# Kernel optimization log

Hardware: AMD Instinct MI355X
Metric: run time of the kernel (lower is better)

## Reference

```python
import jax, jax.numpy as jnp
import numpy as np

DIM = 2048
N_HEADS = 16
HEAD_DIM = DIM // N_HEADS
WINDOW = 256
B, S = 2, 2048


def setup_inputs() -> dict:
    key = jax.random.key(0)
    kx, kq, kk, kv, ko = jax.random.split(key, 5)
    bound = 1.0 / np.sqrt(DIM)  # nn.Linear default init range
    x = jax.random.normal(kx, (B, S, DIM), dtype=jnp.float32)
    wq = jax.random.uniform(kq, (DIM, DIM), jnp.float32, -bound, bound)
    wk = jax.random.uniform(kk, (DIM, DIM), jnp.float32, -bound, bound)
    wv = jax.random.uniform(kv, (DIM, DIM), jnp.float32, -bound, bound)
    wo = jax.random.uniform(ko, (DIM, DIM), jnp.float32, -bound, bound)
    return {"x": x, "wq": wq, "wk": wk, "wv": wv, "wo": wo}


def reference(x, wq, wk, wv, wo):
    b, s, d = x.shape
    scale = HEAD_DIM ** -0.5
    # projections (torch Linear: y = x @ W.T)
    q = (x @ wq.T).reshape(b, s, N_HEADS, HEAD_DIM)
    k = (x @ wk.T).reshape(b, s, N_HEADS, HEAD_DIM)
    v = (x @ wv.T).reshape(b, s, N_HEADS, HEAD_DIM)
    # scores: [b, h, i, j]
    scores = jnp.einsum("bihd,bjhd->bhij", q, k) * scale
    # faithful mask: (all-ones, window cleared, then triu(1)) == mask iff j - i > window//2
    idx = jnp.arange(s)
    mask = (idx[None, :] - idx[:, None]) > (WINDOW // 2)  # [s, s] bool, True = masked
    scores = jnp.where(mask[None, None, :, :], -jnp.inf, scores)
    attn = jax.nn.softmax(scores, axis=-1)
    out = jnp.einsum("bhij,bjhd->bihd", attn, v).reshape(b, s, d)
    return out @ wo.T
```

## Files before the change

### kernel.cpp

```cpp
#include <hip/hip_runtime.h>
#include <stdint.h>
#include <stddef.h>

#define DIMN 2048
#define NH 16
#define HD 128
#define SEQ 2048
#define WIN 128

typedef __attribute__((ext_vector_type(4))) float f32x4;
typedef __attribute__((ext_vector_type(8))) short bf16x8;
typedef __attribute__((ext_vector_type(4))) int i32x4;

__device__ __forceinline__ unsigned short f2bf(float f) {
  union { float f; unsigned u; } v; v.f = f;
  unsigned r = v.u + 0x7FFFu + ((v.u >> 16) & 1u);
  return (unsigned short)(r >> 16);
}

__global__ void cast_bf16_kernel(const float* __restrict__ src,
                                 unsigned short* __restrict__ dst, int n4) {
  int i = blockIdx.x * blockDim.x + threadIdx.x;
  const int stride = gridDim.x * blockDim.x;
  for (; i < n4; i += stride) {
    float4 v = ((const float4*)src)[i];
    ushort4 o;
    o.x = f2bf(v.x); o.y = f2bf(v.y); o.z = f2bf(v.z); o.w = f2bf(v.w);
    ((ushort4*)dst)[i] = o;
  }
}

__global__ void cast4_bf16_kernel(const float* __restrict__ s0, const float* __restrict__ s1,
                                  const float* __restrict__ s2, const float* __restrict__ s3,
                                  unsigned short* __restrict__ dst, int n4) {
  const float* s = (blockIdx.y == 0) ? s0 : (blockIdx.y == 1) ? s1 : (blockIdx.y == 2) ? s2 : s3;
  unsigned short* d = dst + (size_t)blockIdx.y * 4194304;
  int i = blockIdx.x * blockDim.x + threadIdx.x;
  const int stride = gridDim.x * blockDim.x;
  for (; i < n4; i += stride) {
    float4 v = ((const float4*)s)[i];
    ushort4 o;
    o.x = f2bf(v.x); o.y = f2bf(v.y); o.z = f2bf(v.z); o.w = f2bf(v.w);
    ((ushort4*)d)[i] = o;
  }
}

__device__ __forceinline__ void gemm_mainloop_128(
    const unsigned short* __restrict__ A, const unsigned short* __restrict__ B,
    int m0, int n0,
    unsigned short (*As)[40], unsigned short (*Bs)[40],
    f32x4 acc[4][4]) {
  const int t = threadIdx.x;
  const int lane = t & 63, wid = t >> 6;
  const int c = lane & 15, g = lane >> 4;
  const int wr = wid >> 1, wc = wid & 1;
  const int sr = t >> 2;
  const int sc8 = (t & 3) * 8;

  const unsigned short* pa0 = A + (size_t)(m0 + sr) * DIMN + sc8;
  const unsigned short* pa1 = pa0 + (size_t)64 * DIMN;
  const unsigned short* pb0 = B + (size_t)(n0 + sr) * DIMN + sc8;
  const unsigned short* pb1 = pb0 + (size_t)64 * DIMN;

  i32x4 ra0 = *(const i32x4*)pa0;
  i32x4 ra1 = *(const i32x4*)pa1;
  i32x4 rb0 = *(const i32x4*)pb0;
  i32x4 rb1 = *(const i32x4*)pb1;

  for (int k0 = 0; k0 < DIMN; k0 += 32) {
    __syncthreads();
    *(i32x4*)&As[sr][sc8] = ra0;
    *(i32x4*)&As[sr + 64][sc8] = ra1;
    *(i32x4*)&Bs[sr][sc8] = rb0;
    *(i32x4*)&Bs[sr + 64][sc8] = rb1;
    __syncthreads();
    if (k0 + 32 < DIMN) {
      ra0 = *(const i32x4*)(pa0 + k0 + 32);
      ra1 = *(const i32x4*)(pa1 + k0 + 32);
      rb0 = *(const i32x4*)(pb0 + k0 + 32);
      rb1 = *(const i32x4*)(pb1 + k0 + 32);
    }
    bf16x8 af[4], bfv[4];
#pragma unroll
    for (int mi = 0; mi < 4; ++mi)
      af[mi] = *(const bf16x8*)&As[wr * 64 + mi * 16 + c][g * 8];
#pragma unroll
    for (int ni = 0; ni < 4; ++ni)
      bfv[ni] = *(const bf16x8*)&Bs[wc * 64 + ni * 16 + c][g * 8];
#pragma unroll
    for (int mi = 0; mi < 4; ++mi)
#pragma unroll
      for (int ni = 0; ni < 4; ++ni)
        acc[mi][ni] = __builtin_amdgcn_mfma_f32_16x16x32_bf16(
            af[mi], bfv[ni], acc[mi][ni], 0, 0, 0);
  }
}

__global__ __launch_bounds__(256, 2) void gemm_qkv_kernel(
    const unsigned short* __restrict__ Xb,
    const unsigned short* __restrict__ Wq,
    const unsigned short* __restrict__ Wk,
    const unsigned short* __restrict__ Wv,
    unsigned short* __restrict__ Qb,
    unsigned short* __restrict__ Kb,
    unsigned short* __restrict__ Vt) {
  __shared__ __attribute__((aligned(16))) unsigned short As[128][40];
  __shared__ __attribute__((aligned(16))) unsigned short Bs[128][40];
  const int z = blockIdx.z;
  const unsigned short* W = (z == 0) ? Wq : (z == 1) ? Wk : Wv;
  const int m0 = blockIdx.y * 128, n0 = blockIdx.x * 128;

  f32x4 acc[4][4];
  const f32x4 zv = {0.f, 0.f, 0.f, 0.f};
#pragma unroll
  for (int i = 0; i < 4; ++i)
#pragma unroll
    for (int j = 0; j < 4; ++j) acc[i][j] = zv;

  gemm_mainloop_128(Xb, W, m0, n0, As, Bs, acc);

  const int lane = threadIdx.x & 63, wid = threadIdx.x >> 6;
  const int c = lane & 15, g = lane >> 4;
  const int wr = wid >> 1, wc = wid & 1;
  unsigned short* Out01 = (z == 0) ? Qb : Kb;
#pragma unroll
  for (int mi = 0; mi < 4; ++mi) {
#pragma unroll
    for (int ni = 0; ni < 4; ++ni) {
      const int mrow = m0 + wr * 64 + mi * 16 + g * 4;
      const int ncol = n0 + wc * 64 + ni * 16 + c;
      const int h = ncol >> 7, d = ncol & 127;
      const int b = mrow >> 11, s = mrow & 2047;
      if (z < 2) {
#pragma unroll
        for (int j = 0; j < 4; ++j)
          Out01[((size_t)(b * NH + h) * SEQ + s + j) * HD + d] =
              f2bf(acc[mi][ni][j]);
      } else {
        ushort4 pk;
        pk.x = f2bf(acc[mi][ni][0]); pk.y = f2bf(acc[mi][ni][1]);
        pk.z = f2bf(acc[mi][ni][2]); pk.w = f2bf(acc[mi][ni][3]);
        *(ushort4*)&Vt[((size_t)(b * NH + h) * HD + d) * SEQ + s] = pk;
      }
    }
  }
}

__global__ __launch_bounds__(256, 2) void gemm_out_kernel(
    const unsigned short* __restrict__ Ab,
    const unsigned short* __restrict__ Wo,
    float* __restrict__ Cf) {
  __shared__ __attribute__((aligned(16))) unsigned short As[128][40];
  __shared__ __attribute__((aligned(16))) unsigned short Bs[128][40];
  const int m0 = blockIdx.y * 128, n0 = blockIdx.x * 128;

  f32x4 acc[4][4];
  const f32x4 zv = {0.f, 0.f, 0.f, 0.f};
#pragma unroll
  for (int i = 0; i < 4; ++i)
#pragma unroll
    for (int j = 0; j < 4; ++j) acc[i][j] = zv;

  gemm_mainloop_128(Ab, Wo, m0, n0, As, Bs, acc);

  const int lane = threadIdx.x & 63, wid = threadIdx.x >> 6;
  const int c = lane & 15, g = lane >> 4;
  const int wr = wid >> 1, wc = wid & 1;
#pragma unroll
  for (int mi = 0; mi < 4; ++mi) {
#pragma unroll
    for (int ni = 0; ni < 4; ++ni) {
      const int mrow = m0 + wr * 64 + mi * 16 + g * 4;
      const int ncol = n0 + wc * 64 + ni * 16 + c;
#pragma unroll
      for (int j = 0; j < 4; ++j)
        Cf[(size_t)(mrow + j) * DIMN + ncol] = acc[mi][ni][j];
    }
  }
}

__global__ __launch_bounds__(256, 2) void attn_kernel(
    const unsigned short* __restrict__ Qg,
    const unsigned short* __restrict__ Kg,
    const unsigned short* __restrict__ Vtg,
    unsigned short* __restrict__ Og) {
  __shared__ __attribute__((aligned(16))) unsigned short Ks[64 * 128];
  __shared__ __attribute__((aligned(16))) unsigned short Vs[128 * 64];
  __shared__ __attribute__((aligned(16))) unsigned short Ps[4 * 32 * 64];

  const int bh = blockIdx.x, qt = blockIdx.y;
  const int q0 = qt * 128;
  const int t = threadIdx.x, wid = t >> 6, lane = t & 63;
  const int c = lane & 15, g = lane >> 4;
  const int swc = c & 7;

  const unsigned short* Kbh = Kg + (size_t)bh * SEQ * HD;
  const unsigned short* Vbh = Vtg + (size_t)bh * HD * SEQ;

  bf16x8 qf[2][4];
#pragma unroll
  for (int mi = 0; mi < 2; ++mi) {
    const unsigned short* qb =
        Qg + ((size_t)bh * SEQ + q0 + wid * 32 + mi * 16 + c) * HD + g * 8;
#pragma unroll
    for (int kk = 0; kk < 4; ++kk) qf[mi][kk] = *(const bf16x8*)(qb + kk * 32);
  }

  f32x4 o[2][8];
  const f32x4 zv = {0.f, 0.f, 0.f, 0.f};
#pragma unroll
  for (int mi = 0; mi < 2; ++mi)
#pragma unroll
    for (int ni = 0; ni < 8; ++ni) o[mi][ni] = zv;
  float M[2][4], L[2][4];
#pragma unroll
  for (int mi = 0; mi < 2; ++mi)
#pragma unroll
    for (int j = 0; j < 4; ++j) { M[mi][j] = -1e30f; L[mi][j] = 0.f; }

  const int ntA = (q0 + 256) >> 6;
  const int nt = (ntA < (SEQ >> 6)) ? ntA : (SEQ >> 6);
  const float kl2e = 0.08838834764831845f * 1.4426950408889634f;

  const int kswz = (t & 15) ^ ((t >> 4) & 7);
  const int vswz = (t & 7) ^ ((t >> 3) & 7);
  const int kgo = (t >> 4) * HD + (t & 15) * 8;
  const int klo = (t >> 4) * 128 + kswz * 8;
  const int vlo = (t >> 3) * 64 + vswz * 8;
  const size_t vgo = (size_t)(t >> 3) * SEQ + (t & 7) * 8;

  i32x4 kc[4], vc[4];
#pragma unroll
  for (int r = 0; r < 4; ++r) {
    kc[r] = *(const i32x4*)(Kbh + (size_t)r * 16 * HD + kgo);
    vc[r] = *(const i32x4*)(Vbh + (size_t)r * 32 * SEQ + vgo);
  }

  for (int tt = 0; tt < nt; ++tt) {
    const int j0 = tt * 64;
    __syncthreads();
#pragma unroll
    for (int r = 0; r < 4; ++r) {
      *(i32x4*)&Ks[r * 2048 + klo] = kc[r];
      *(i32x4*)&Vs[r * 2048 + vlo] = vc[r];
    }
    __syncthreads();
    if (tt + 1 < nt) {
      const int j1 = j0 + 64;
#pragma unroll
      for (int r = 0; r < 4; ++r) {
        kc[r] = *(const i32x4*)(Kbh + (size_t)(j1 + r * 16) * HD + kgo);
        vc[r] = *(const i32x4*)(Vbh + (size_t)r * 32 * SEQ + j1 + vgo);
      }
    }

    f32x4 sc[2][4];
#pragma unroll
    for (int mi = 0; mi < 2; ++mi)
#pragma unroll
      for (int ni = 0; ni < 4; ++ni) sc[mi][ni] = zv;
#pragma unroll
    for (int kk = 0; kk < 4; ++kk) {
#pragma unroll
      for (int ni = 0; ni < 4; ++ni) {
        const bf16x8 kf =
            *(const bf16x8*)&Ks[(ni * 16 + c) * 128 + ((kk * 4 + g) ^ swc) * 8];
        sc[0][ni] = __builtin_amdgcn_mfma_f32_16x16x32_bf16(qf[0][kk], kf, sc[0][ni], 0, 0, 0);
        sc[1][ni] = __builtin_amdgcn_mfma_f32_16x16x32_bf16(qf[1][kk], kf, sc[1][ni], 0, 0, 0);
      }
    }

    if (j0 - q0 >= 128) {
#pragma unroll
      for (int mi = 0; mi < 2; ++mi)
#pragma unroll
        for (int ni = 0; ni < 4; ++ni) {
          const int jg = j0 + ni * 16 + c;
#pragma unroll
          for (int j = 0; j < 4; ++j) {
            const int ig = q0 + wid * 32 + mi * 16 + g * 4 + j;
            if (jg > ig + WIN) sc[mi][ni][j] = -3.0e38f;
          }
        }
    }

    float tmax[2][4], dmax = -3.0e38f;
#pragma unroll
    for (int mi = 0; mi < 2; ++mi)
#pragma unroll
      for (int j = 0; j < 4; ++j) {
        float mx = fmaxf(fmaxf(sc[mi][0][j], sc[mi][1][j]),
                         fmaxf(sc[mi][2][j], sc[mi][3][j]));
        mx = fmaxf(mx, __shfl_xor(mx, 1));
        mx = fmaxf(mx, __shfl_xor(mx, 2));
        mx = fmaxf(mx, __shfl_xor(mx, 4));
        mx = fmaxf(mx, __shfl_xor(mx, 8));
        tmax[mi][j] = mx;
        dmax = fmaxf(dmax, mx - M[mi][j]);
      }
    if (__any(dmax > 64.f)) {
#pragma unroll
      for (int mi = 0; mi < 2; ++mi)
#pragma unroll
        for (int j = 0; j < 4; ++j) {
          const float nm = fmaxf(M[mi][j], tmax[mi][j]);
          const float al = __builtin_amdgcn_exp2f((M[mi][j] - nm) * kl2e);
          M[mi][j] = nm;
          L[mi][j] *= al;
#pragma unroll
          for (int ni = 0; ni < 8; ++ni) o[mi][ni][j] *= al;
        }
    }

    float rs[2][4] = {{0.f, 0.f, 0.f, 0.f}, {0.f, 0.f, 0.f, 0.f}};
#pragma unroll
    for (int mi = 0; mi < 2; ++mi)
#pragma unroll
      for (int ni = 0; ni < 4; ++ni)
#pragma unroll
        for (int j = 0; j < 4; ++j) {
          const float p = __builtin_amdgcn_exp2f((sc[mi][ni][j] - M[mi][j]) * kl2e);
          rs[mi][j] += p;
          const int prow = mi * 16 + g * 4 + j;
          Ps[wid * 2048 + prow * 64 + ((2 * ni + (c >> 3)) ^ (prow & 7)) * 8 + (c & 7)] =
              f2bf(p);
        }
#pragma unroll
    for (int mi = 0; mi < 2; ++mi)
#pragma unroll
      for (int j = 0; j < 4; ++j) {
        float s = rs[mi][j];
        s += __shfl_xor(s, 1);
        s += __shfl_xor(s, 2);
        s += __shfl_xor(s, 4);
        s += __shfl_xor(s, 8);
        L[mi][j] += s;
      }

#pragma unroll
    for (int kk2 = 0; kk2 < 2; ++kk2) {
      bf16x8 pf[2];
#pragma unroll
      for (int mi = 0; mi < 2; ++mi)
        pf[mi] = *(const bf16x8*)&Ps[wid * 2048 + (mi * 16 + c) * 64 +
                                     ((kk2 * 4 + g) ^ swc) * 8];
#pragma unroll
      for (int ni = 0; ni < 8; ++ni) {
        const bf16x8 vf =
            *(const bf16x8*)&Vs[(ni * 16 + c) * 64 + ((kk2 * 4 + g) ^ swc) * 8];
        o[0][ni] = __builtin_amdgcn_mfma_f32_16x16x32_bf16(pf[0], vf, o[0][ni], 0, 0, 0);
        o[1][ni] = __builtin_amdgcn_mfma_f32_16x16x32_bf16(pf[1], vf, o[1][ni], 0, 0, 0);
      }
    }
  }

  const int b = bh >> 4, h = bh & 15;
#pragma unroll
  for (int mi = 0; mi < 2; ++mi)
#pragma unroll
    for (int j = 0; j < 4; ++j) {
      const float inv = 1.0f / L[mi][j];
      const int s = q0 + wid * 32 + mi * 16 + g * 4 + j;
      unsigned short* orow = Og + (size_t)(b * SEQ + s) * DIMN + h * HD;
#pragma unroll
      for (int ni = 0; ni < 8; ++ni) orow[ni * 16 + c] = f2bf(o[mi][ni][j] * inv);
    }
}

extern "C" void kernel_launch(void* const* d_in, const int* in_sizes, int n_in,
                              void* d_out, int out_size, void* d_ws, size_t ws_size,
                              hipStream_t stream) {
  (void)in_sizes; (void)n_in; (void)out_size; (void)ws_size;
  const float* x  = (const float*)d_in[0];
  const float* wq = (const float*)d_in[1];
  const float* wk = (const float*)d_in[2];
  const float* wv = (const float*)d_in[3];
  const float* wo = (const float*)d_in[4];
  float* out = (float*)d_out;

  unsigned short* xb  = (unsigned short*)d_ws;
  unsigned short* wqb = xb  + (size_t)8388608;
  unsigned short* wkb = wqb + (size_t)4194304;
  unsigned short* wvb = wkb + (size_t)4194304;
  unsigned short* wob = wvb + (size_t)4194304;
  unsigned short* Qb  = wob + (size_t)4194304;
  unsigned short* Kb  = Qb  + (size_t)8388608;
  unsigned short* Vt  = Kb  + (size_t)8388608;
  unsigned short* Ab  = Vt  + (size_t)8388608;

  cast_bf16_kernel<<<dim3(1024), dim3(256), 0, stream>>>(x, xb, 2097152);
  cast4_bf16_kernel<<<dim3(512, 4), dim3(256), 0, stream>>>(wq, wk, wv, wo, wqb, 1048576);

  gemm_qkv_kernel<<<dim3(16, 32, 3), dim3(256), 0, stream>>>(xb, wqb, wkb, wvb, Qb, Kb, Vt);
  attn_kernel<<<dim3(32, 16), dim3(256), 0, stream>>>(Qb, Kb, Vt, Ab);
  gemm_out_kernel<<<dim3(16, 32), dim3(256), 0, stream>>>(Ab, wob, out);
}
```

Measured before the change: 417.4 us.

## Use direct global-to-LDS loads with swizzled tiles in GEMMs, reorder attention tiles, add priorities

The GEMM mainloop now stages tiles with global_load_lds straight into XOR-swizzled LDS tiles, uses a K step of 64 instead of 32, and raises the occupancy hint to 3 blocks. The goal is to cut the register round-trip and LDS bank conflicts in staging. The attention kernel remaps query tile indices so tiles with different amounts of work are interleaved in launch order, and raises wave priority around the MFMA sections. In exchange, the GEMM loses its register prefetch overlap: each iteration now loads and then waits behind a barrier with no double buffering.

```diff
diff --git a/kernel.cpp b/kernel.cpp
--- a/kernel.cpp
+++ b/kernel.cpp
@@ -11,6 +11,9 @@
 typedef __attribute__((ext_vector_type(4))) float f32x4;
 typedef __attribute__((ext_vector_type(8))) short bf16x8;
 typedef __attribute__((ext_vector_type(4))) int i32x4;
+
+#define AS1 __attribute__((address_space(1)))
+#define AS3 __attribute__((address_space(3)))
 
 __device__ __forceinline__ unsigned short f2bf(float f) {
   union { float f; unsigned u; } v; v.f = f;
@@ -45,58 +48,56 @@
   }
 }
 
-__device__ __forceinline__ void gemm_mainloop_128(
+__device__ __forceinline__ void gemm_mainloop_g128(
     const unsigned short* __restrict__ A, const unsigned short* __restrict__ B,
-    int m0, int n0,
-    unsigned short (*As)[40], unsigned short (*Bs)[40],
-    f32x4 acc[4][4]) {
-  const int t = threadIdx.x;
-  const int lane = t & 63, wid = t >> 6;
+    int m0, int n0, unsigned short* As, unsigned short* Bs, f32x4 acc[4][4]) {
+  const int t = threadIdx.x, lane = t & 63, wid = t >> 6;
   const int c = lane & 15, g = lane >> 4;
   const int wr = wid >> 1, wc = wid & 1;
-  const int sr = t >> 2;
-  const int sc8 = (t & 3) * 8;
-
-  const unsigned short* pa0 = A + (size_t)(m0 + sr) * DIMN + sc8;
-  const unsigned short* pa1 = pa0 + (size_t)64 * DIMN;
-  const unsigned short* pb0 = B + (size_t)(n0 + sr) * DIMN + sc8;
-  const unsigned short* pb1 = pb0 + (size_t)64 * DIMN;
-
-  i32x4 ra0 = *(const i32x4*)pa0;
-  i32x4 ra1 = *(const i32x4*)pa1;
-  i32x4 rb0 = *(const i32x4*)pb0;
-  i32x4 rb1 = *(const i32x4*)pb1;
-
-  for (int k0 = 0; k0 < DIMN; k0 += 32) {
+
+  const int srow = wid * 32 + (lane >> 3);
+  const int gslot = (lane & 7) ^ (lane >> 3);
+  const unsigned short* ga = A + (size_t)(m0 + srow) * DIMN + gslot * 8;
+  const unsigned short* gb = B + (size_t)(n0 + srow) * DIMN + gslot * 8;
+  unsigned short* la = As + (size_t)(wid * 32) * 64;
+  unsigned short* lb = Bs + (size_t)(wid * 32) * 64;
+
+  const int swc = c & 7;
+
+  for (int k0 = 0; k0 < DIMN; k0 += 64) {
     __syncthreads();
-    *(i32x4*)&As[sr][sc8] = ra0;
-    *(i32x4*)&As[sr + 64][sc8] = ra1;
-    *(i32x4*)&Bs[sr][sc8] = rb0;
-    *(i32x4*)&Bs[sr + 64][sc8] = rb1;
+#pragma unroll
+    for (int i = 0; i < 4; ++i) {
+      __builtin_amdgcn_global_load_lds(
+          (const AS1 unsigned*)(ga + (size_t)i * 8 * DIMN + k0),
+          (AS3 unsigned*)(la + i * 8 * 64), 16, 0, 0);
+      __builtin_amdgcn_global_load_lds(
+          (const AS1 unsigned*)(gb + (size_t)i * 8 * DIMN + k0),
+          (AS3 unsigned*)(lb + i * 8 * 64), 16, 0, 0);
+    }
     __syncthreads();
-    if (k0 + 32 < DIMN) {
-      ra0 = *(const i32x4*)(pa0 + k0 + 32);
-      ra1 = *(const i32x4*)(pa1 + k0 + 32);
-      rb0 = *(const i32x4*)(pb0 + k0 + 32);
-      rb1 = *(const i32x4*)(pb1 + k0 + 32);
-    }
-    bf16x8 af[4], bfv[4];
-#pragma unroll
-    for (int mi = 0; mi < 4; ++mi)
-      af[mi] = *(const bf16x8*)&As[wr * 64 + mi * 16 + c][g * 8];
-#pragma unroll
-    for (int ni = 0; ni < 4; ++ni)
-      bfv[ni] = *(const bf16x8*)&Bs[wc * 64 + ni * 16 + c][g * 8];
-#pragma unroll
-    for (int mi = 0; mi < 4; ++mi)
+#pragma unroll
+    for (int kk = 0; kk < 2; ++kk) {
+      bf16x8 af[4], bfv[4];
+#pragma unroll
+      for (int mi = 0; mi < 4; ++mi)
+        af[mi] = *(const bf16x8*)&As[(wr * 64 + mi * 16 + c) * 64 +
+                                     (((kk * 4 + g) ^ swc) * 8)];
 #pragma unroll
       for (int ni = 0; ni < 4; ++ni)
-        acc[mi][ni] = __builtin_amdgcn_mfma_f32_16x16x32_bf16(
-            af[mi], bfv[ni], acc[mi][ni], 0, 0, 0);
-  }
-}
-
-__global__ __launch_bounds__(256, 2) void gemm_qkv_kernel(
+        bfv[ni] = *(const bf16x8*)&Bs[(wc * 64 + ni * 16 + c) * 64 +
+                                      (((kk * 4 + g) ^ swc) * 8)];
+#pragma unroll
+      for (int mi = 0; mi < 4; ++mi)
+#pragma unroll
+        for (int ni = 0; ni < 4; ++ni)
+          acc[mi][ni] = __builtin_amdgcn_mfma_f32_16x16x32_bf16(
+              af[mi], bfv[ni], acc[mi][ni], 0, 0, 0);
+    }
+  }
+}
+
+__global__ __launch_bounds__(256, 3) void gemm_qkv_kernel(
     const unsigned short* __restrict__ Xb,
     const unsigned short* __restrict__ Wq,
     const unsigned short* __restrict__ Wk,
@@ -104,8 +105,8 @@
     unsigned short* __restrict__ Qb,
     unsigned short* __restrict__ Kb,
     unsigned short* __restrict__ Vt) {
-  __shared__ __attribute__((aligned(16))) unsigned short As[128][40];
-  __shared__ __attribute__((aligned(16))) unsigned short Bs[128][40];
+  __shared__ __attribute__((aligned(16))) unsigned short As[128 * 64];
+  __shared__ __attribute__((aligned(16))) unsigned short Bs[128 * 64];
   const int z = blockIdx.z;
   const unsigned short* W = (z == 0) ? Wq : (z == 1) ? Wk : Wv;
   const int m0 = blockIdx.y * 128, n0 = blockIdx.x * 128;
@@ -117,7 +118,7 @@
 #pragma unroll
     for (int j = 0; j < 4; ++j) acc[i][j] = zv;
 
-  gemm_mainloop_128(Xb, W, m0, n0, As, Bs, acc);
+  gemm_mainloop_g128(Xb, W, m0, n0, As, Bs, acc);
 
   const int lane = threadIdx.x & 63, wid = threadIdx.x >> 6;
   const int c = lane & 15, g = lane >> 4;
@@ -146,12 +147,12 @@
   }
 }
 
-__global__ __launch_bounds__(256, 2) void gemm_out_kernel(
+__global__ __launch_bounds__(256, 3) void gemm_out_kernel(
     const unsigned short* __restrict__ Ab,
     const unsigned short* __restrict__ Wo,
     float* __restrict__ Cf) {
-  __shared__ __attribute__((aligned(16))) unsigned short As[128][40];
-  __shared__ __attribute__((aligned(16))) unsigned short Bs[128][40];
+  __shared__ __attribute__((aligned(16))) unsigned short As[128 * 64];
+  __shared__ __attribute__((aligned(16))) unsigned short Bs[128 * 64];
   const int m0 = blockIdx.y * 128, n0 = blockIdx.x * 128;
 
   f32x4 acc[4][4];
@@ -161,7 +162,7 @@
 #pragma unroll
     for (int j = 0; j < 4; ++j) acc[i][j] = zv;
 
-  gemm_mainloop_128(Ab, Wo, m0, n0, As, Bs, acc);
+  gemm_mainloop_g128(Ab, Wo, m0, n0, As, Bs, acc);
 
   const int lane = threadIdx.x & 63, wid = threadIdx.x >> 6;
   const int c = lane & 15, g = lane >> 4;
@@ -188,7 +189,9 @@
   __shared__ __attribute__((aligned(16))) unsigned short Vs[128 * 64];
   __shared__ __attribute__((aligned(16))) unsigned short Ps[4 * 32 * 64];
 
-  const int bh = blockIdx.x, qt = blockIdx.y;
+  const int bh = blockIdx.x;
+  const int yy = blockIdx.y;
+  const int qt = (yy < 8) ? yy : 23 - yy;
   const int q0 = qt * 128;
   const int t = threadIdx.x, wid = t >> 6, lane = t & 63;
   const int c = lane & 15, g = lane >> 4;
@@ -259,6 +262,7 @@
     for (int mi = 0; mi < 2; ++mi)
 #pragma unroll
       for (int ni = 0; ni < 4; ++ni) sc[mi][ni] = zv;
+    __builtin_amdgcn_s_setprio(1);
 #pragma unroll
     for (int kk = 0; kk < 4; ++kk) {
 #pragma unroll
@@ -269,6 +273,7 @@
         sc[1][ni] = __builtin_amdgcn_mfma_f32_16x16x32_bf16(qf[1][kk], kf, sc[1][ni], 0, 0, 0);
       }
     }
+    __builtin_amdgcn_s_setprio(0);
 
     if (j0 - q0 >= 128) {
 #pragma unroll
@@ -337,6 +342,7 @@
         L[mi][j] += s;
       }
 
+    __builtin_amdgcn_s_setprio(1);
 #pragma unroll
     for (int kk2 = 0; kk2 < 2; ++kk2) {
       bf16x8 pf[2];
@@ -352,6 +358,7 @@
         o[1][ni] = __builtin_amdgcn_mfma_f32_16x16x32_bf16(pf[1], vf, o[1][ni], 0, 0, 0);
       }
     }
+    __builtin_amdgcn_s_setprio(0);
   }
 
   const int b = bh >> 4, h = bh & 15;
```

New measurement: 376.1 us. 9.9% less time.
